# Performance work log

Hardware: AMD Instinct MI355X
Metric: run time of the kernel (lower is better)

Reference implementation:

```python
import jax, jax.numpy as jnp
import numpy as np

N = 25000   # nodes
E = 600000  # edges (multiple of 48)
IN, H, OUT = 128, 256, 128
SLOPE = 0.01  # LeakyReLU default negative_slope


def _lin(x, w, b):
    return x @ w.T + b


def _leaky(v):
    return jnp.where(v > 0, v, SLOPE * v)


def _sage(x, src, dst, lw, lb, rw):
    # PyG SAGEConv (aggr='mean', root_weight=True, normalize=False):
    # out = lin_l(mean_{j in N(i)} x_j) + lin_r(x_i)
    agg = jax.ops.segment_sum(x[src], dst, num_segments=N)
    deg = jax.ops.segment_sum(jnp.ones((src.shape[0],), x.dtype), dst, num_segments=N)
    mean = agg / jnp.maximum(deg, 1.0)[:, None]
    return mean @ lw.T + lb + x @ rw.T


def setup_inputs() -> dict:
    key = jax.random.key(0)
    ks = jax.random.split(key, 32)

    def w(k, o, i):
        return jax.random.normal(k, (o, i), jnp.float32) * (1.0 / np.sqrt(i))

    def b(k, o):
        return jax.random.normal(k, (o,), jnp.float32) * 0.01

    inp = {
        'x': jax.random.normal(ks[0], (N, IN), jnp.float32),
        'edge_index': jax.random.randint(ks[1], (2, E), 0, N, dtype=jnp.int32),
        'edge_attr': jax.random.normal(ks[2], (E, 1), jnp.float32),
        'batch': jnp.zeros((N,), jnp.int32),
        'prelin_w': w(ks[3], H, IN), 'prelin_b': b(ks[4], H),
        'conv1_lw': w(ks[5], H, H), 'conv1_lb': b(ks[6], H), 'conv1_rw': w(ks[7], H, H),
        'conv2_lw': w(ks[8], H, H), 'conv2_lb': b(ks[9], H), 'conv2_rw': w(ks[10], H, H),
        'conv3_lw': w(ks[11], OUT, H), 'conv3_lb': b(ks[12], OUT), 'conv3_rw': w(ks[13], OUT, H),
        'hh1_w': w(ks[14], H, H), 'hh1_b': b(ks[15], H),
        'hh2_w': w(ks[16], H, H), 'hh2_b': b(ks[17], H),
        'oo_w': w(ks[18], OUT, OUT), 'oo_b': b(ks[19], OUT),
        'lin96_w': w(ks[20], 1, 192), 'lin96_b': b(ks[21], 1),
        'lin32_w': w(ks[22], 1, 64), 'lin32_b': b(ks[23], 1),
    }
    return inp


def reference(x, edge_index, edge_attr, batch,
              prelin_w, prelin_b,
              conv1_lw, conv1_lb, conv1_rw,
              conv2_lw, conv2_lb, conv2_rw,
              conv3_lw, conv3_lb, conv3_rw,
              hh1_w, hh1_b, hh2_w, hh2_b,
              oo_w, oo_b, lin96_w, lin96_b, lin32_w, lin32_b):
    src, dst = edge_index[0], edge_index[1]
    h = jax.nn.relu(_lin(x, prelin_w, prelin_b))
    h = jax.nn.relu(_sage(h, src, dst, conv1_lw, conv1_lb, conv1_rw))
    h = _leaky(_lin(h, hh1_w, hh1_b))
    h = jax.nn.relu(_sage(h, src, dst, conv2_lw, conv2_lb, conv2_rw))
    h = _leaky(_lin(h, hh2_w, hh2_b))
    h = jax.nn.relu(_sage(h, src, dst, conv3_lw, conv3_lb, conv3_rw))
    h = _leaky(_lin(h, oo_w, oo_b))  # [N, 128]

    xl = h[src]  # edge_left  = edge_index[0]
    xr = h[dst]  # edge_right = edge_index[1]
    f96 = jnp.concatenate([xl[:, :96], xr[:, :96]], axis=1)  # [E, 192]
    f32 = jnp.concatenate([xl[:, 96:], xr[:, 96:]], axis=1)  # [E, 64]
    f96 = jax.nn.relu(_lin(f96, lin96_w, lin96_b))  # [E, 1]
    f32 = jax.nn.relu(_lin(f32, lin32_w, lin32_b))  # [E, 1]
    edge_out = f96 * edge_attr + f32                # [E, 1]
    edge_out = edge_out.reshape(-1, 48).mean(axis=1).reshape(-1, 1)  # [E/48, 1]
    return edge_out
```

## Files before the change

kernel.cpp:

```cpp
#include <hip/hip_runtime.h>
#include <hip/hip_bf16.h>

#define N_NODES 25000
#define N_EDGES 600000
#define ACT_NONE 0
#define ACT_RELU 1
#define ACT_LEAKY 2

typedef __bf16 bf16x8 __attribute__((ext_vector_type(8)));
typedef float f32x4 __attribute__((ext_vector_type(4)));
typedef unsigned short u16x8 __attribute__((ext_vector_type(8)));
typedef unsigned short u16x4 __attribute__((ext_vector_type(4)));
typedef short s16x4 __attribute__((ext_vector_type(4)));

__device__ __forceinline__ unsigned short f2bf(float x) {
    union { float f; unsigned int u; } v; v.f = x;
    unsigned int r = (v.u + 0x7fffu + ((v.u >> 16) & 1u)) >> 16;
    return (unsigned short)r;
}
__device__ __forceinline__ float bf2f(unsigned short b) {
    union { float f; unsigned int u; } v; v.u = ((unsigned int)b) << 16;
    return v.f;
}

__global__ __launch_bounds__(256) void hist_kernel(const int* __restrict__ dst,
                                                   int* __restrict__ deg, int E) {
    int e = blockIdx.x * 256 + threadIdx.x;
    if (e < E) atomicAdd(&deg[dst[e]], 1);
}

__global__ __launch_bounds__(1024) void scan_kernel(const int* __restrict__ deg,
                                                    int* __restrict__ off,
                                                    int* __restrict__ cursor, int n) {
    __shared__ int wsum[16];
    int t = threadIdx.x, w = t >> 6, l = t & 63;
    int carry = 0;
    for (int base = 0; base < n; base += 1024) {
        int v = (base + t < n) ? deg[base + t] : 0;
        int x = v;
        #pragma unroll
        for (int d = 1; d < 64; d <<= 1) {
            int y = __shfl_up(x, d);
            if (l >= d) x += y;
        }
        if (l == 63) wsum[w] = x;
        __syncthreads();
        if (w == 0 && l < 16) {
            int s = wsum[l];
            #pragma unroll
            for (int d = 1; d < 16; d <<= 1) {
                int y = __shfl_up(s, d);
                if (l >= d) s += y;
            }
            wsum[l] = s;
        }
        __syncthreads();
        int woff = (w > 0) ? wsum[w - 1] : 0;
        int excl = x + woff - v;
        if (base + t < n) {
            off[base + t] = carry + excl;
            cursor[base + t] = carry + excl;
        }
        int total = wsum[15];
        __syncthreads();
        carry += total;
    }
    if (t == 0) off[n] = carry;
}

__global__ __launch_bounds__(256) void scatter_kernel(const int* __restrict__ src,
                                                      const int* __restrict__ dst,
                                                      int* __restrict__ cursor,
                                                      int* __restrict__ csr_src, int E) {
    int e = blockIdx.x * 256 + threadIdx.x;
    if (e < E) {
        int d = dst[e];
        int pos = atomicAdd(&cursor[d], 1);
        csr_src[pos] = src[e];
    }
}

__global__ __launch_bounds__(256) void convert_kernel(const float* __restrict__ src,
                                                      unsigned short* __restrict__ hi,
                                                      unsigned short* __restrict__ lo, int n) {
    int i = blockIdx.x * 256 + threadIdx.x;
    if (i < n) {
        float x = src[i];
        unsigned short h = f2bf(x);
        hi[i] = h;
        lo[i] = f2bf(x - bf2f(h));
    }
}

struct CvtBatch {
    const float* src[10];
    unsigned short* hi[10];
    unsigned short* lo[10];
    int count[10];
};
__global__ __launch_bounds__(256) void convert_batch_kernel(CvtBatch b) {
    int seg = blockIdx.y;
    int n = b.count[seg];
    int i = blockIdx.x * 256 + threadIdx.x;
    if (i >= n) return;
    float x = b.src[seg][i];
    unsigned short h = f2bf(x);
    b.hi[seg][i] = h;
    b.lo[seg][i] = f2bf(x - bf2f(h));
}

__global__ __launch_bounds__(256) void quant_kernel(const float* __restrict__ h,
                                                    short* __restrict__ qt,
                                                    float* __restrict__ qscale) {
    int node = blockIdx.x * 4 + (threadIdx.x >> 6);
    if (node >= N_NODES) return;
    int lane = threadIdx.x & 63;
    long base = (long)node * 256 + (long)lane * 4;
    f32x4 v = *(const f32x4*)&h[base];
    float m = fmaxf(fmaxf(fabsf(v[0]), fabsf(v[1])), fmaxf(fabsf(v[2]), fabsf(v[3])));
    #pragma unroll
    for (int d = 32; d > 0; d >>= 1) m = fmaxf(m, __shfl_xor(m, d));
    float inv = (m > 0.0f) ? 32767.0f / m : 0.0f;
    float scale = (m > 0.0f) ? m / 32767.0f : 0.0f;
    s16x4 q;
    #pragma unroll
    for (int j = 0; j < 4; ++j) q[j] = (short)(int)rintf(v[j] * inv);
    *(s16x4*)&qt[base] = q;
    if (lane == 0) qscale[node] = scale;
}

__global__ __launch_bounds__(256) void sage_mean_kernel(const short* __restrict__ qt,
                                                        const float* __restrict__ qscale,
                                                        const int* __restrict__ off,
                                                        const int* __restrict__ csr_src,
                                                        unsigned short* __restrict__ mh,
                                                        unsigned short* __restrict__ ml) {
    int node = blockIdx.x * 4 + (threadIdx.x >> 6);
    if (node >= N_NODES) return;
    int lane = threadIdx.x & 63;
    int s0 = off[node], s1 = off[node + 1];
    f32x4 acc0 = {0.f, 0.f, 0.f, 0.f}, acc1 = {0.f, 0.f, 0.f, 0.f};
    f32x4 acc2 = {0.f, 0.f, 0.f, 0.f}, acc3 = {0.f, 0.f, 0.f, 0.f};
    long loff = (long)lane * 4;
    int e = s0;
    for (; e + 4 <= s1; e += 4) {
        int iA = csr_src[e], iB = csr_src[e + 1], iC = csr_src[e + 2], iD = csr_src[e + 3];
        s16x4 qa = *(const s16x4*)&qt[(long)iA * 256 + loff];
        s16x4 qb = *(const s16x4*)&qt[(long)iB * 256 + loff];
        s16x4 qc = *(const s16x4*)&qt[(long)iC * 256 + loff];
        s16x4 qd = *(const s16x4*)&qt[(long)iD * 256 + loff];
        float sa = qscale[iA], sb = qscale[iB], sc = qscale[iC], sd = qscale[iD];
        #pragma unroll
        for (int j = 0; j < 4; ++j) {
            acc0[j] += sa * (float)qa[j];
            acc1[j] += sb * (float)qb[j];
            acc2[j] += sc * (float)qc[j];
            acc3[j] += sd * (float)qd[j];
        }
    }
    for (; e < s1; ++e) {
        int iA = csr_src[e];
        s16x4 qa = *(const s16x4*)&qt[(long)iA * 256 + loff];
        float sa = qscale[iA];
        #pragma unroll
        for (int j = 0; j < 4; ++j) acc0[j] += sa * (float)qa[j];
    }
    float inv = 1.0f / fmaxf((float)(s1 - s0), 1.0f);
    f32x4 m = ((acc0 + acc1) + (acc2 + acc3)) * inv;
    u16x4 hb, lb;
    #pragma unroll
    for (int j = 0; j < 4; ++j) {
        unsigned short hv = f2bf(m[j]);
        hb[j] = hv;
        lb[j] = f2bf(m[j] - bf2f(hv));
    }
    long base = (long)node * 256 + loff;
    *(u16x4*)&mh[base] = hb;
    *(u16x4*)&ml[base] = lb;
}

__global__ __launch_bounds__(256, 2) void gemm_mfma_kernel(
    const unsigned short* __restrict__ A1h, const unsigned short* __restrict__ A1l,
    const unsigned short* __restrict__ W1h, const unsigned short* __restrict__ W1l,
    const unsigned short* __restrict__ A2h, const unsigned short* __restrict__ A2l,
    const unsigned short* __restrict__ W2h, const unsigned short* __restrict__ W2l,
    const float* __restrict__ bias,
    float* __restrict__ Cf, unsigned short* __restrict__ Ch, unsigned short* __restrict__ Cl,
    int M, int K, int O, int act)
{
    __shared__ unsigned short sAh[128][32];
    __shared__ unsigned short sAl[128][32];
    __shared__ unsigned short sWh[128][32];
    __shared__ unsigned short sWl[128][32];

    int tid = threadIdx.x;
    int row0 = blockIdx.x * 128;
    int col0 = blockIdx.y * 128;
    int wid = tid >> 6, lane = tid & 63;
    int wm = (wid >> 1) * 64, wo = (wid & 1) * 64;
    int fr = lane & 15, qk = lane >> 4;

    int rr = lane >> 2, qq = lane & 3;

    f32x4 acc[4][4] = {};

    for (int pass = 0; pass < 2; ++pass) {
        const unsigned short* Ah = pass ? A2h : A1h;
        const unsigned short* Al = pass ? A2l : A1l;
        const unsigned short* Wh = pass ? W2h : W1h;
        const unsigned short* Wl = pass ? W2l : W1l;
        if (Ah == nullptr) continue;
        for (int k0 = 0; k0 < K; k0 += 32) {
            #pragma unroll
            for (int i = 0; i < 2; ++i) {
                int rb = wid * 32 + i * 16;
                int r = rb + rr;
                int gc = ((qq + (r >> 1)) & 3) * 8;
                long ar = (long)(row0 + r);
                if (ar > M - 1) ar = M - 1;
                long wr = (long)(col0 + r);
                const unsigned short* pAh = Ah + ar * K + k0 + gc;
                const unsigned short* pAl = Al + ar * K + k0 + gc;
                const unsigned short* pWh = Wh + wr * K + k0 + gc;
                const unsigned short* pWl = Wl + wr * K + k0 + gc;
                __builtin_amdgcn_global_load_lds(
                    (const __attribute__((address_space(1))) unsigned int*)pAh,
                    (__attribute__((address_space(3))) unsigned int*)&sAh[rb][0], 16, 0, 0);
                __builtin_amdgcn_global_load_lds(
                    (const __attribute__((address_space(1))) unsigned int*)pAl,
                    (__attribute__((address_space(3))) unsigned int*)&sAl[rb][0], 16, 0, 0);
                __builtin_amdgcn_global_load_lds(
                    (const __attribute__((address_space(1))) unsigned int*)pWh,
                    (__attribute__((address_space(3))) unsigned int*)&sWh[rb][0], 16, 0, 0);
                __builtin_amdgcn_global_load_lds(
                    (const __attribute__((address_space(1))) unsigned int*)pWl,
                    (__attribute__((address_space(3))) unsigned int*)&sWl[rb][0], 16, 0, 0);
            }
            __syncthreads();

            bf16x8 ah[4], al[4], bh[4], bl[4];
            #pragma unroll
            for (int i = 0; i < 4; ++i) {
                int rowA = wm + i * 16 + fr;
                int offA = rowA * 32 + 8 * ((qk - (rowA >> 1)) & 3);
                ah[i] = *(const bf16x8*)(&sAh[0][0] + offA);
                al[i] = *(const bf16x8*)(&sAl[0][0] + offA);
                int rowB = wo + i * 16 + fr;
                int offB = rowB * 32 + 8 * ((qk - (rowB >> 1)) & 3);
                bh[i] = *(const bf16x8*)(&sWh[0][0] + offB);
                bl[i] = *(const bf16x8*)(&sWl[0][0] + offB);
            }
            #pragma unroll
            for (int i = 0; i < 4; ++i) {
                #pragma unroll
                for (int j = 0; j < 4; ++j) {
                    acc[i][j] = __builtin_amdgcn_mfma_f32_16x16x32_bf16(ah[i], bh[j], acc[i][j], 0, 0, 0);
                    acc[i][j] = __builtin_amdgcn_mfma_f32_16x16x32_bf16(ah[i], bl[j], acc[i][j], 0, 0, 0);
                    acc[i][j] = __builtin_amdgcn_mfma_f32_16x16x32_bf16(al[i], bh[j], acc[i][j], 0, 0, 0);
                }
            }
            __syncthreads();
        }
    }

    int rgrp = (lane >> 4) * 4;
    int cl_ = lane & 15;
    #pragma unroll
    for (int i = 0; i < 4; ++i) {
        #pragma unroll
        for (int j = 0; j < 4; ++j) {
            int gcol = col0 + wo + j * 16 + cl_;
            float bv = bias[gcol];
            #pragma unroll
            for (int r = 0; r < 4; ++r) {
                int grow = row0 + wm + i * 16 + rgrp + r;
                if (grow < M) {
                    float v = acc[i][j][r] + bv;
                    if (act == ACT_RELU)       v = fmaxf(v, 0.0f);
                    else if (act == ACT_LEAKY) v = (v > 0.0f) ? v : 0.01f * v;
                    long idx = (long)grow * O + gcol;
                    if (Cf) Cf[idx] = v;
                    if (Ch) {
                        unsigned short hbits = f2bf(v);
                        Ch[idx] = hbits;
                        Cl[idx] = f2bf(v - bf2f(hbits));
                    }
                }
            }
        }
    }
}

__global__ __launch_bounds__(256) void node_dots_kernel(const float* __restrict__ h,
                                                        const float* __restrict__ w96,
                                                        const float* __restrict__ w32,
                                                        float* __restrict__ nodeDot) {
    int node = blockIdx.x * 4 + (threadIdx.x >> 6);
    if (node >= N_NODES) return;
    int lane = threadIdx.x & 63;
    const float* row = h + (long)node * 128;
    float h0 = row[lane];
    float h1 = row[64 + lane];
    float pL96 = h0 * w96[lane];
    float pR96 = h0 * w96[96 + lane];
    float pL32 = 0.0f, pR32 = 0.0f;
    if (lane < 32) {
        pL96 += h1 * w96[64 + lane];
        pR96 += h1 * w96[160 + lane];
    } else {
        int k = lane - 32;
        pL32 = h1 * w32[k];
        pR32 = h1 * w32[32 + k];
    }
    #pragma unroll
    for (int m = 32; m > 0; m >>= 1) {
        pL96 += __shfl_xor(pL96, m);
        pR96 += __shfl_xor(pR96, m);
        pL32 += __shfl_xor(pL32, m);
        pR32 += __shfl_xor(pR32, m);
    }
    if (lane == 0) {
        f32x4 v = {pL96, pR96, pL32, pR32};
        *(f32x4*)&nodeDot[(long)node * 4] = v;
    }
}

__global__ __launch_bounds__(256) void edge_aff_kernel(const float* __restrict__ nodeDot,
                                                       const int* __restrict__ src,
                                                       const int* __restrict__ dst,
                                                       const float* __restrict__ eattr,
                                                       const float* __restrict__ b96,
                                                       const float* __restrict__ b32,
                                                       float* __restrict__ vals, int E) {
    int e = blockIdx.x * 256 + threadIdx.x;
    if (e >= E) return;
    f32x4 a = *(const f32x4*)&nodeDot[(long)src[e] * 4];
    f32x4 b = *(const f32x4*)&nodeDot[(long)dst[e] * 4];
    float f96  = fmaxf(a[0] + b[1] + b96[0], 0.0f);
    float f32v = fmaxf(a[2] + b[3] + b32[0], 0.0f);
    vals[e] = f96 * eattr[e] + f32v;
}

__global__ __launch_bounds__(256) void group_mean_kernel(const float* __restrict__ vals,
                                                         float* __restrict__ out, int G) {
    int g = blockIdx.x * 256 + threadIdx.x;
    if (g >= G) return;
    float s = 0.0f;
    #pragma unroll
    for (int k = 0; k < 48; ++k) s += vals[g * 48 + k];
    out[g] = s * (1.0f / 48.0f);
}

extern "C" void kernel_launch(void* const* d_in, const int* in_sizes, int n_in,
                              void* d_out, int out_size, void* d_ws, size_t ws_size,
                              hipStream_t stream) {
    const float* x         = (const float*)d_in[0];
    const int*   edge_idx  = (const int*)d_in[1];
    const float* edge_attr = (const float*)d_in[2];
    const float* prelin_w  = (const float*)d_in[4];
    const float* prelin_b  = (const float*)d_in[5];
    const float* conv1_lw  = (const float*)d_in[6];
    const float* conv1_lb  = (const float*)d_in[7];
    const float* conv1_rw  = (const float*)d_in[8];
    const float* conv2_lw  = (const float*)d_in[9];
    const float* conv2_lb  = (const float*)d_in[10];
    const float* conv2_rw  = (const float*)d_in[11];
    const float* conv3_lw  = (const float*)d_in[12];
    const float* conv3_lb  = (const float*)d_in[13];
    const float* conv3_rw  = (const float*)d_in[14];
    const float* hh1_w     = (const float*)d_in[15];
    const float* hh1_b     = (const float*)d_in[16];
    const float* hh2_w     = (const float*)d_in[17];
    const float* hh2_b     = (const float*)d_in[18];
    const float* oo_w      = (const float*)d_in[19];
    const float* oo_b      = (const float*)d_in[20];
    const float* lin96_w   = (const float*)d_in[21];
    const float* lin96_b   = (const float*)d_in[22];
    const float* lin32_w   = (const float*)d_in[23];
    const float* lin32_b   = (const float*)d_in[24];

    const int* src = edge_idx;
    const int* dst = edge_idx + N_EDGES;

    char* wsp = (char*)d_ws;
    size_t used = 0;
    auto alloc = [&](size_t bytes) -> char* {
        char* r = wsp;
        size_t pad = (bytes + 255) & ~(size_t)255;
        wsp += pad; used += pad;
        return r;
    };
    float* bufF = (float*)alloc((size_t)N_NODES * 256 * 4);
    unsigned short* P0h = (unsigned short*)alloc((size_t)N_NODES * 256 * 2);
    unsigned short* P0l = (unsigned short*)alloc((size_t)N_NODES * 256 * 2);
    unsigned short* P1h = (unsigned short*)alloc((size_t)N_NODES * 256 * 2);
    unsigned short* P1l = (unsigned short*)alloc((size_t)N_NODES * 256 * 2);
    unsigned short* P2h = (unsigned short*)alloc((size_t)N_NODES * 256 * 2);
    unsigned short* P2l = (unsigned short*)alloc((size_t)N_NODES * 256 * 2);
    short* qtab    = (short*)alloc((size_t)N_NODES * 256 * 2);
    float* qscale  = (float*)alloc((size_t)N_NODES * 4);
    float* evals   = (float*)alloc((size_t)N_EDGES * 4);
    float* nodeDot = (float*)alloc((size_t)N_NODES * 4 * 4);
    int* deg       = (int*)alloc((size_t)N_NODES * 4);
    int* off       = (int*)alloc((size_t)(N_NODES + 1) * 4);
    int* cursor    = (int*)alloc((size_t)N_NODES * 4);
    int* csr_src   = (int*)alloc((size_t)N_EDGES * 4);

    struct WP { unsigned short *h, *l; };
    auto wpair = [&](int n) -> WP {
        WP w; w.h = (unsigned short*)alloc((size_t)n * 2);
        w.l = (unsigned short*)alloc((size_t)n * 2); return w;
    };
    WP w_pre = wpair(256 * 128);
    WP w_c1l = wpair(256 * 256), w_c1r = wpair(256 * 256);
    WP w_c2l = wpair(256 * 256), w_c2r = wpair(256 * 256);
    WP w_c3l = wpair(128 * 256), w_c3r = wpair(128 * 256);
    WP w_h1  = wpair(256 * 256), w_h2 = wpair(256 * 256);
    WP w_oo  = wpair(128 * 128);

    if (used > ws_size) return;

    const int EB = (N_EDGES + 255) / 256;
    const int MB = (N_NODES + 127) / 128;
    const int NB4 = (N_NODES + 3) / 4;

    (void)hipMemsetAsync(deg, 0, N_NODES * sizeof(int), stream);
    hist_kernel<<<EB, 256, 0, stream>>>(dst, deg, N_EDGES);
    scan_kernel<<<1, 1024, 0, stream>>>(deg, off, cursor, N_NODES);
    scatter_kernel<<<EB, 256, 0, stream>>>(src, dst, cursor, csr_src, N_EDGES);

    convert_kernel<<<((N_NODES * 128) + 255) / 256, 256, 0, stream>>>(x, P0h, P0l, N_NODES * 128);
    CvtBatch cb;
    const float* wsrc[10] = {prelin_w, conv1_lw, conv1_rw, conv2_lw, conv2_rw,
                             conv3_lw, conv3_rw, hh1_w, hh2_w, oo_w};
    WP wdst[10] = {w_pre, w_c1l, w_c1r, w_c2l, w_c2r, w_c3l, w_c3r, w_h1, w_h2, w_oo};
    int wcnt[10] = {256 * 128, 256 * 256, 256 * 256, 256 * 256, 256 * 256,
                    128 * 256, 128 * 256, 256 * 256, 256 * 256, 128 * 128};
    for (int i = 0; i < 10; ++i) {
        cb.src[i] = wsrc[i]; cb.hi[i] = wdst[i].h; cb.lo[i] = wdst[i].l; cb.count[i] = wcnt[i];
    }
    convert_batch_kernel<<<dim3((65536 + 255) / 256, 10), 256, 0, stream>>>(cb);

    gemm_mfma_kernel<<<dim3(MB, 2), 256, 0, stream>>>(
        P0h, P0l, w_pre.h, w_pre.l, nullptr, nullptr, nullptr, nullptr,
        prelin_b, bufF, P1h, P1l, N_NODES, 128, 256, ACT_RELU);

    quant_kernel<<<NB4, 256, 0, stream>>>(bufF, qtab, qscale);
    sage_mean_kernel<<<NB4, 256, 0, stream>>>(qtab, qscale, off, csr_src, P2h, P2l);
    gemm_mfma_kernel<<<dim3(MB, 2), 256, 0, stream>>>(
        P2h, P2l, w_c1l.h, w_c1l.l, P1h, P1l, w_c1r.h, w_c1r.l,
        conv1_lb, nullptr, P0h, P0l, N_NODES, 256, 256, ACT_RELU);
    gemm_mfma_kernel<<<dim3(MB, 2), 256, 0, stream>>>(
        P0h, P0l, w_h1.h, w_h1.l, nullptr, nullptr, nullptr, nullptr,
        hh1_b, bufF, P1h, P1l, N_NODES, 256, 256, ACT_LEAKY);

    quant_kernel<<<NB4, 256, 0, stream>>>(bufF, qtab, qscale);
    sage_mean_kernel<<<NB4, 256, 0, stream>>>(qtab, qscale, off, csr_src, P2h, P2l);
    gemm_mfma_kernel<<<dim3(MB, 2), 256, 0, stream>>>(
        P2h, P2l, w_c2l.h, w_c2l.l, P1h, P1l, w_c2r.h, w_c2r.l,
        conv2_lb, nullptr, P0h, P0l, N_NODES, 256, 256, ACT_RELU);
    gemm_mfma_kernel<<<dim3(MB, 2), 256, 0, stream>>>(
        P0h, P0l, w_h2.h, w_h2.l, nullptr, nullptr, nullptr, nullptr,
        hh2_b, bufF, P1h, P1l, N_NODES, 256, 256, ACT_LEAKY);

    quant_kernel<<<NB4, 256, 0, stream>>>(bufF, qtab, qscale);
    sage_mean_kernel<<<NB4, 256, 0, stream>>>(qtab, qscale, off, csr_src, P2h, P2l);
    gemm_mfma_kernel<<<dim3(MB, 1), 256, 0, stream>>>(
        P2h, P2l, w_c3l.h, w_c3l.l, P1h, P1l, w_c3r.h, w_c3r.l,
        conv3_lb, nullptr, P0h, P0l, N_NODES, 256, 128, ACT_RELU);
    gemm_mfma_kernel<<<dim3(MB, 1), 256, 0, stream>>>(
        P0h, P0l, w_oo.h, w_oo.l, nullptr, nullptr, nullptr, nullptr,
        oo_b, bufF, nullptr, nullptr, N_NODES, 128, 128, ACT_LEAKY);

    node_dots_kernel<<<NB4, 256, 0, stream>>>(bufF, lin96_w, lin32_w, nodeDot);
    edge_aff_kernel<<<EB, 256, 0, stream>>>(nodeDot, src, dst, edge_attr,
                                            lin96_b, lin32_b, evals, N_EDGES);
    const int G = N_EDGES / 48;
    group_mean_kernel<<<(G + 255) / 256, 256, 0, stream>>>(evals, (float*)d_out, G);
}
```

Baseline: 483.1 us.

## Double-buffer LDS tiles in split-bf16 MFMA GEMM to overlap loads with compute

Doubles the shared-memory tile buffers and restructures the GEMM K-loop so the next tile is prefetched into the alternate buffer while MFMAs run on the current one. The two passes (root and neighbour weights) are merged into one flat tile loop, and each iteration needs one barrier instead of two. This aims to hide global-to-LDS load latency, but doubles LDS use to 64KB per block, which may limit occupancy under the 2-blocks-per-SM launch bound. The loads are async global_load_lds and the code relies on a single barrier per iteration to order them; no explicit vmcnt wait is added, so correctness depends on how the barrier handles outstanding loads.

```diff
diff --git a/kernel.cpp b/kernel.cpp
--- a/kernel.cpp
+++ b/kernel.cpp
@@ -188,10 +188,10 @@
     float* __restrict__ Cf, unsigned short* __restrict__ Ch, unsigned short* __restrict__ Cl,
     int M, int K, int O, int act)
 {
-    __shared__ unsigned short sAh[128][32];
-    __shared__ unsigned short sAl[128][32];
-    __shared__ unsigned short sWh[128][32];
-    __shared__ unsigned short sWl[128][32];
+    __shared__ unsigned short sAh[2][128][32];
+    __shared__ unsigned short sAl[2][128][32];
+    __shared__ unsigned short sWh[2][128][32];
+    __shared__ unsigned short sWl[2][128][32];
 
     int tid = threadIdx.x;
     int row0 = blockIdx.x * 128;
@@ -199,68 +199,70 @@
     int wid = tid >> 6, lane = tid & 63;
     int wm = (wid >> 1) * 64, wo = (wid & 1) * 64;
     int fr = lane & 15, qk = lane >> 4;
-
     int rr = lane >> 2, qq = lane & 3;
 
+    const int nt1 = K >> 5;
+    const int nt  = (A2h != nullptr) ? (nt1 << 1) : nt1;
+
     f32x4 acc[4][4] = {};
 
-    for (int pass = 0; pass < 2; ++pass) {
-        const unsigned short* Ah = pass ? A2h : A1h;
-        const unsigned short* Al = pass ? A2l : A1l;
-        const unsigned short* Wh = pass ? W2h : W1h;
-        const unsigned short* Wl = pass ? W2l : W1l;
-        if (Ah == nullptr) continue;
-        for (int k0 = 0; k0 < K; k0 += 32) {
+    auto STAGE = [&](int buf, int t) {
+        const unsigned short *Ah, *Al, *Wh, *Wl;
+        int k0;
+        if (t < nt1) { Ah = A1h; Al = A1l; Wh = W1h; Wl = W1l; k0 = t << 5; }
+        else         { Ah = A2h; Al = A2l; Wh = W2h; Wl = W2l; k0 = (t - nt1) << 5; }
+        #pragma unroll
+        for (int i = 0; i < 2; ++i) {
+            int rb = wid * 32 + i * 16;
+            int r = rb + rr;
+            int gc = ((qq + (r >> 1)) & 3) * 8;
+            long ar = (long)(row0 + r);
+            if (ar > M - 1) ar = M - 1;
+            long wr = (long)(col0 + r);
+            __builtin_amdgcn_global_load_lds(
+                (const __attribute__((address_space(1))) unsigned int*)(Ah + ar * K + k0 + gc),
+                (__attribute__((address_space(3))) unsigned int*)&sAh[buf][rb][0], 16, 0, 0);
+            __builtin_amdgcn_global_load_lds(
+                (const __attribute__((address_space(1))) unsigned int*)(Al + ar * K + k0 + gc),
+                (__attribute__((address_space(3))) unsigned int*)&sAl[buf][rb][0], 16, 0, 0);
+            __builtin_amdgcn_global_load_lds(
+                (const __attribute__((address_space(1))) unsigned int*)(Wh + wr * K + k0 + gc),
+                (__attribute__((address_space(3))) unsigned int*)&sWh[buf][rb][0], 16, 0, 0);
+            __builtin_amdgcn_global_load_lds(
+                (const __attribute__((address_space(1))) unsigned int*)(Wl + wr * K + k0 + gc),
+                (__attribute__((address_space(3))) unsigned int*)&sWl[buf][rb][0], 16, 0, 0);
+        }
+    };
+
+    STAGE(0, 0);
+    __syncthreads();
+
+    for (int t = 0; t < nt; ++t) {
+        int cur = t & 1;
+        if (t + 1 < nt) STAGE(cur ^ 1, t + 1);
+
+        bf16x8 ah[4], al[4], bh[4], bl[4];
+        #pragma unroll
+        for (int i = 0; i < 4; ++i) {
+            int rowA = wm + i * 16 + fr;
+            int offA = rowA * 32 + 8 * ((qk - (rowA >> 1)) & 3);
+            ah[i] = *(const bf16x8*)(&sAh[cur][0][0] + offA);
+            al[i] = *(const bf16x8*)(&sAl[cur][0][0] + offA);
+            int rowB = wo + i * 16 + fr;
+            int offB = rowB * 32 + 8 * ((qk - (rowB >> 1)) & 3);
+            bh[i] = *(const bf16x8*)(&sWh[cur][0][0] + offB);
+            bl[i] = *(const bf16x8*)(&sWl[cur][0][0] + offB);
+        }
+        #pragma unroll
+        for (int i = 0; i < 4; ++i) {
             #pragma unroll
-            for (int i = 0; i < 2; ++i) {
-                int rb = wid * 32 + i * 16;
-                int r = rb + rr;
-                int gc = ((qq + (r >> 1)) & 3) * 8;
-                long ar = (long)(row0 + r);
-                if (ar > M - 1) ar = M - 1;
-                long wr = (long)(col0 + r);
-                const unsigned short* pAh = Ah + ar * K + k0 + gc;
-                const unsigned short* pAl = Al + ar * K + k0 + gc;
-                const unsigned short* pWh = Wh + wr * K + k0 + gc;
-                const unsigned short* pWl = Wl + wr * K + k0 + gc;
-                __builtin_amdgcn_global_load_lds(
-                    (const __attribute__((address_space(1))) unsigned int*)pAh,
-                    (__attribute__((address_space(3))) unsigned int*)&sAh[rb][0], 16, 0, 0);
-                __builtin_amdgcn_global_load_lds(
-                    (const __attribute__((address_space(1))) unsigned int*)pAl,
-                    (__attribute__((address_space(3))) unsigned int*)&sAl[rb][0], 16, 0, 0);
-                __builtin_amdgcn_global_load_lds(
-                    (const __attribute__((address_space(1))) unsigned int*)pWh,
-                    (__attribute__((address_space(3))) unsigned int*)&sWh[rb][0], 16, 0, 0);
-                __builtin_amdgcn_global_load_lds(
-                    (const __attribute__((address_space(1))) unsigned int*)pWl,
-                    (__attribute__((address_space(3))) unsigned int*)&sWl[rb][0], 16, 0, 0);
+            for (int j = 0; j < 4; ++j) {
+                acc[i][j] = __builtin_amdgcn_mfma_f32_16x16x32_bf16(ah[i], bh[j], acc[i][j], 0, 0, 0);
+                acc[i][j] = __builtin_amdgcn_mfma_f32_16x16x32_bf16(ah[i], bl[j], acc[i][j], 0, 0, 0);
+                acc[i][j] = __builtin_amdgcn_mfma_f32_16x16x32_bf16(al[i], bh[j], acc[i][j], 0, 0, 0);
             }
-            __syncthreads();
-
-            bf16x8 ah[4], al[4], bh[4], bl[4];
-            #pragma unroll
-            for (int i = 0; i < 4; ++i) {
-                int rowA = wm + i * 16 + fr;
-                int offA = rowA * 32 + 8 * ((qk - (rowA >> 1)) & 3);
-                ah[i] = *(const bf16x8*)(&sAh[0][0] + offA);
-                al[i] = *(const bf16x8*)(&sAl[0][0] + offA);
-                int rowB = wo + i * 16 + fr;
-                int offB = rowB * 32 + 8 * ((qk - (rowB >> 1)) & 3);
-                bh[i] = *(const bf16x8*)(&sWh[0][0] + offB);
-                bl[i] = *(const bf16x8*)(&sWl[0][0] + offB);
-            }
-            #pragma unroll
-            for (int i = 0; i < 4; ++i) {
-                #pragma unroll
-                for (int j = 0; j < 4; ++j) {
-                    acc[i][j] = __builtin_amdgcn_mfma_f32_16x16x32_bf16(ah[i], bh[j], acc[i][j], 0, 0, 0);
-                    acc[i][j] = __builtin_amdgcn_mfma_f32_16x16x32_bf16(ah[i], bl[j], acc[i][j], 0, 0, 0);
-                    acc[i][j] = __builtin_amdgcn_mfma_f32_16x16x32_bf16(al[i], bh[j], acc[i][j], 0, 0, 0);
-                }
-            }
-            __syncthreads();
-        }
+        }
+        __syncthreads();
     }
 
     int rgrp = (lane >> 4) * 4;
```

New measurement: 487.5 us. Within noise of the previous version (+0.9%).

## Double GEMM K-tile to 64 and fuse edge scoring with group mean

Applied to the files above, without the earlier changes.

The MFMA GEMM now stages 64-wide K tiles in LDS instead of 32, with both passes merged into one flat tile loop. This halves the barrier and loop overhead per K element at the cost of doubling LDS use, which may reduce occupancy. Separately, the per-edge affine kernel and the 48-edge group mean are fused into one kernel so the intermediate edge-values buffer is never written or read. The fused kernel runs only 12.5k threads with strided, uncoalesced per-thread loops, so it may use the GPU poorly.

```diff
diff --git a/kernel.cpp b/kernel.cpp
--- a/kernel.cpp
+++ b/kernel.cpp
@@ -188,10 +188,10 @@
     float* __restrict__ Cf, unsigned short* __restrict__ Ch, unsigned short* __restrict__ Cl,
     int M, int K, int O, int act)
 {
-    __shared__ unsigned short sAh[128][32];
-    __shared__ unsigned short sAl[128][32];
-    __shared__ unsigned short sWh[128][32];
-    __shared__ unsigned short sWl[128][32];
+    __shared__ unsigned short sAh[128][64];
+    __shared__ unsigned short sAl[128][64];
+    __shared__ unsigned short sWh[128][64];
+    __shared__ unsigned short sWl[128][64];
 
     int tid = threadIdx.x;
     int row0 = blockIdx.x * 128;
@@ -199,54 +199,53 @@
     int wid = tid >> 6, lane = tid & 63;
     int wm = (wid >> 1) * 64, wo = (wid & 1) * 64;
     int fr = lane & 15, qk = lane >> 4;
-
-    int rr = lane >> 2, qq = lane & 3;
+    int rr = lane >> 3, qq = lane & 7;
+    int shalf = (qq >> 2) * 32, scq = qq & 3;
+
+    const int nt1 = K >> 6;
+    const int nt  = (A2h != nullptr) ? (nt1 << 1) : nt1;
 
     f32x4 acc[4][4] = {};
 
-    for (int pass = 0; pass < 2; ++pass) {
-        const unsigned short* Ah = pass ? A2h : A1h;
-        const unsigned short* Al = pass ? A2l : A1l;
-        const unsigned short* Wh = pass ? W2h : W1h;
-        const unsigned short* Wl = pass ? W2l : W1l;
-        if (Ah == nullptr) continue;
-        for (int k0 = 0; k0 < K; k0 += 32) {
-            #pragma unroll
-            for (int i = 0; i < 2; ++i) {
-                int rb = wid * 32 + i * 16;
-                int r = rb + rr;
-                int gc = ((qq + (r >> 1)) & 3) * 8;
-                long ar = (long)(row0 + r);
-                if (ar > M - 1) ar = M - 1;
-                long wr = (long)(col0 + r);
-                const unsigned short* pAh = Ah + ar * K + k0 + gc;
-                const unsigned short* pAl = Al + ar * K + k0 + gc;
-                const unsigned short* pWh = Wh + wr * K + k0 + gc;
-                const unsigned short* pWl = Wl + wr * K + k0 + gc;
-                __builtin_amdgcn_global_load_lds(
-                    (const __attribute__((address_space(1))) unsigned int*)pAh,
-                    (__attribute__((address_space(3))) unsigned int*)&sAh[rb][0], 16, 0, 0);
-                __builtin_amdgcn_global_load_lds(
-                    (const __attribute__((address_space(1))) unsigned int*)pAl,
-                    (__attribute__((address_space(3))) unsigned int*)&sAl[rb][0], 16, 0, 0);
-                __builtin_amdgcn_global_load_lds(
-                    (const __attribute__((address_space(1))) unsigned int*)pWh,
-                    (__attribute__((address_space(3))) unsigned int*)&sWh[rb][0], 16, 0, 0);
-                __builtin_amdgcn_global_load_lds(
-                    (const __attribute__((address_space(1))) unsigned int*)pWl,
-                    (__attribute__((address_space(3))) unsigned int*)&sWl[rb][0], 16, 0, 0);
-            }
-            __syncthreads();
-
+    for (int t = 0; t < nt; ++t) {
+        const unsigned short *Ah, *Al, *Wh, *Wl;
+        int k0;
+        if (t < nt1) { Ah = A1h; Al = A1l; Wh = W1h; Wl = W1l; k0 = t << 6; }
+        else         { Ah = A2h; Al = A2l; Wh = W2h; Wl = W2l; k0 = (t - nt1) << 6; }
+
+        #pragma unroll
+        for (int i = 0; i < 4; ++i) {
+            int rb = wid * 32 + i * 8;
+            int r  = rb + rr;
+            int gs = shalf + ((scq + (r >> 1)) & 3) * 8;
+            long ar = (long)(row0 + r); if (ar > M - 1) ar = M - 1;
+            long wr = (long)(col0 + r);
+            __builtin_amdgcn_global_load_lds(
+                (const __attribute__((address_space(1))) unsigned int*)(Ah + ar * K + k0 + gs),
+                (__attribute__((address_space(3))) unsigned int*)&sAh[rb][0], 16, 0, 0);
+            __builtin_amdgcn_global_load_lds(
+                (const __attribute__((address_space(1))) unsigned int*)(Al + ar * K + k0 + gs),
+                (__attribute__((address_space(3))) unsigned int*)&sAl[rb][0], 16, 0, 0);
+            __builtin_amdgcn_global_load_lds(
+                (const __attribute__((address_space(1))) unsigned int*)(Wh + wr * K + k0 + gs),
+                (__attribute__((address_space(3))) unsigned int*)&sWh[rb][0], 16, 0, 0);
+            __builtin_amdgcn_global_load_lds(
+                (const __attribute__((address_space(1))) unsigned int*)(Wl + wr * K + k0 + gs),
+                (__attribute__((address_space(3))) unsigned int*)&sWl[rb][0], 16, 0, 0);
+        }
+        __syncthreads();
+
+        #pragma unroll
+        for (int kk = 0; kk < 2; ++kk) {
             bf16x8 ah[4], al[4], bh[4], bl[4];
             #pragma unroll
             for (int i = 0; i < 4; ++i) {
                 int rowA = wm + i * 16 + fr;
-                int offA = rowA * 32 + 8 * ((qk - (rowA >> 1)) & 3);
+                int offA = rowA * 64 + kk * 32 + 8 * ((qk - (rowA >> 1)) & 3);
                 ah[i] = *(const bf16x8*)(&sAh[0][0] + offA);
                 al[i] = *(const bf16x8*)(&sAl[0][0] + offA);
                 int rowB = wo + i * 16 + fr;
-                int offB = rowB * 32 + 8 * ((qk - (rowB >> 1)) & 3);
+                int offB = rowB * 64 + kk * 32 + 8 * ((qk - (rowB >> 1)) & 3);
                 bh[i] = *(const bf16x8*)(&sWh[0][0] + offB);
                 bl[i] = *(const bf16x8*)(&sWl[0][0] + offB);
             }
@@ -259,8 +258,8 @@
                     acc[i][j] = __builtin_amdgcn_mfma_f32_16x16x32_bf16(al[i], bh[j], acc[i][j], 0, 0, 0);
                 }
             }
-            __syncthreads();
-        }
+        }
+        __syncthreads();
     }
 
     int rgrp = (lane >> 4) * 4;
@@ -325,29 +324,27 @@
     }
 }
 
-__global__ __launch_bounds__(256) void edge_aff_kernel(const float* __restrict__ nodeDot,
-                                                       const int* __restrict__ src,
-                                                       const int* __restrict__ dst,
-                                                       const float* __restrict__ eattr,
-                                                       const float* __restrict__ b96,
-                                                       const float* __restrict__ b32,
-                                                       float* __restrict__ vals, int E) {
-    int e = blockIdx.x * 256 + threadIdx.x;
-    if (e >= E) return;
-    f32x4 a = *(const f32x4*)&nodeDot[(long)src[e] * 4];
-    f32x4 b = *(const f32x4*)&nodeDot[(long)dst[e] * 4];
-    float f96  = fmaxf(a[0] + b[1] + b96[0], 0.0f);
-    float f32v = fmaxf(a[2] + b[3] + b32[0], 0.0f);
-    vals[e] = f96 * eattr[e] + f32v;
-}
-
-__global__ __launch_bounds__(256) void group_mean_kernel(const float* __restrict__ vals,
+__global__ __launch_bounds__(256) void edge_group_kernel(const float* __restrict__ nodeDot,
+                                                         const int* __restrict__ src,
+                                                         const int* __restrict__ dst,
+                                                         const float* __restrict__ eattr,
+                                                         const float* __restrict__ b96,
+                                                         const float* __restrict__ b32,
                                                          float* __restrict__ out, int G) {
     int g = blockIdx.x * 256 + threadIdx.x;
     if (g >= G) return;
+    float bb96 = b96[0], bb32 = b32[0];
+    int base = g * 48;
     float s = 0.0f;
-    #pragma unroll
-    for (int k = 0; k < 48; ++k) s += vals[g * 48 + k];
+    #pragma unroll 4
+    for (int k = 0; k < 48; ++k) {
+        int e = base + k;
+        f32x4 a = *(const f32x4*)&nodeDot[(long)src[e] * 4];
+        f32x4 b = *(const f32x4*)&nodeDot[(long)dst[e] * 4];
+        float f96  = fmaxf(a[0] + b[1] + bb96, 0.0f);
+        float f32v = fmaxf(a[2] + b[3] + bb32, 0.0f);
+        s += f96 * eattr[e] + f32v;
+    }
     out[g] = s * (1.0f / 48.0f);
 }
 
@@ -399,7 +396,6 @@
     unsigned short* P2l = (unsigned short*)alloc((size_t)N_NODES * 256 * 2);
     short* qtab    = (short*)alloc((size_t)N_NODES * 256 * 2);
     float* qscale  = (float*)alloc((size_t)N_NODES * 4);
-    float* evals   = (float*)alloc((size_t)N_EDGES * 4);
     float* nodeDot = (float*)alloc((size_t)N_NODES * 4 * 4);
     int* deg       = (int*)alloc((size_t)N_NODES * 4);
     int* off       = (int*)alloc((size_t)(N_NODES + 1) * 4);
@@ -473,8 +469,7 @@
         oo_b, bufF, nullptr, nullptr, N_NODES, 128, 128, ACT_LEAKY);
 
     node_dots_kernel<<<NB4, 256, 0, stream>>>(bufF, lin96_w, lin32_w, nodeDot);
-    edge_aff_kernel<<<EB, 256, 0, stream>>>(nodeDot, src, dst, edge_attr,
-                                            lin96_b, lin32_b, evals, N_EDGES);
     const int G = N_EDGES / 48;
-    group_mean_kernel<<<(G + 255) / 256, 256, 0, stream>>>(evals, (float*)d_out, G);
-}
+    edge_group_kernel<<<(G + 255) / 256, 256, 0, stream>>>(
+        nodeDot, src, dst, edge_attr, lin96_b, lin32_b, (float*)d_out, G);
+}
```

New measurement: 478.2 us. About the same (-1.0%).
